# Kernel optimization log

Hardware: AMD Instinct MI355X
Metric: run time of the kernel (lower is better)

## Reference

```python
import jax, jax.numpy as jnp
import numpy as np

N_NODES = 10000
N_EDGES = 120000
F_IN = 66
HEADS = 10
F_HEAD = 66          # GATConv(66, 66, heads=10) -> concat 660
GCN_OUT = F_IN * HEADS * 2  # 1320


def leaky(x, slope):
    return jnp.where(x >= 0, x, slope * x)


def add_self_loops(edge_index, n):
    loops = jnp.arange(n, dtype=edge_index.dtype)
    src = jnp.concatenate([edge_index[0], loops])
    dst = jnp.concatenate([edge_index[1], loops])
    return src, dst


def gat_conv(x, src, dst, W, att_src, att_dst, bias, n):
    # x: [N, F_IN]; W: [F_IN, HEADS*F_HEAD]
    xt = (x @ W).reshape(n, HEADS, F_HEAD)
    a_s = jnp.sum(xt * att_src, axis=-1)   # [N, H]
    a_d = jnp.sum(xt * att_dst, axis=-1)   # [N, H]
    e = leaky(a_s[src] + a_d[dst], 0.2)    # [E, H]
    # segment softmax over destination nodes
    m = jax.ops.segment_max(e, dst, num_segments=n)
    m = jnp.where(jnp.isfinite(m), m, 0.0)
    ex = jnp.exp(e - m[dst])
    s = jax.ops.segment_sum(ex, dst, num_segments=n)
    alpha = ex / jnp.maximum(s[dst], 1e-16)        # [E, H]
    msg = xt[src] * alpha[:, :, None]              # [E, H, F_HEAD]
    out = jax.ops.segment_sum(msg, dst, num_segments=n)
    return out.reshape(n, HEADS * F_HEAD) + bias


def gcn_conv(x, src, dst, W, b, n):
    xt = x @ W                                     # [N, GCN_OUT]
    ones = jnp.ones(src.shape[0], dtype=xt.dtype)
    deg = jax.ops.segment_sum(ones, dst, num_segments=n)
    dinv = jax.lax.rsqrt(jnp.maximum(deg, 1.0))
    norm = dinv[src] * dinv[dst]                   # [E]
    out = jax.ops.segment_sum(xt[src] * norm[:, None], dst, num_segments=n)
    return out + b


def setup_inputs() -> dict:
    key = jax.random.key(0)
    ks = jax.random.split(key, 16)
    x = jax.random.normal(ks[0], (N_NODES, F_IN), dtype=jnp.float32)
    edge_index = jax.random.randint(ks[1], (2, N_EDGES), 0, N_NODES, dtype=jnp.int32)
    sc = 0.05
    p = {
        'x': x,
        'edge_index': edge_index,
        'W_gat': jax.random.normal(ks[2], (F_IN, HEADS * F_HEAD)) * sc,
        'att_src': jax.random.normal(ks[3], (HEADS, F_HEAD)) * sc,
        'att_dst': jax.random.normal(ks[4], (HEADS, F_HEAD)) * sc,
        'b_gat': jnp.zeros((HEADS * F_HEAD,), jnp.float32),
        'W_gcn': jax.random.normal(ks[5], (HEADS * F_HEAD, GCN_OUT)) * sc,
        'b_gcn': jnp.zeros((GCN_OUT,), jnp.float32),
        'W_g1': jax.random.normal(ks[6], (GCN_OUT, 1000)) * sc,
        'b_g1': jnp.zeros((1000,), jnp.float32),
        'W_g2': jax.random.normal(ks[7], (1000, 64)) * sc,
        'b_g2': jnp.zeros((64,), jnp.float32),
        'W_fc1': jax.random.normal(ks[8], (64, 32)) * sc,
        'b_fc1': jnp.zeros((32,), jnp.float32),
        'W_fc2': jax.random.normal(ks[9], (32, 16)) * sc,
        'b_fc2': jnp.zeros((16,), jnp.float32),
        'W_out': jax.random.normal(ks[10], (16, 1)) * sc,
        'b_out': jnp.zeros((1,), jnp.float32),
    }
    return p


def reference(x, edge_index, W_gat, att_src, att_dst, b_gat, W_gcn, b_gcn,
              W_g1, b_g1, W_g2, b_g2, W_fc1, b_fc1, W_fc2, b_fc2, W_out, b_out):
    n = x.shape[0]
    src, dst = add_self_loops(edge_index, n)
    h = gat_conv(x, src, dst, W_gat, att_src, att_dst, b_gat, n)
    h = leaky(h, 0.01)
    h = gcn_conv(h, src, dst, W_gcn, b_gcn, n)
    h = leaky(h, 0.01)
    h = leaky(h @ W_g1 + b_g1, 0.01)   # dropout = identity (eval)
    h = h @ W_g2 + b_g2
    h = leaky(h, 0.01)
    h = leaky(h @ W_fc1 + b_fc1, 0.01)
    h = leaky(h @ W_fc2 + b_fc2, 0.01)
    return h @ W_out + b_out
```

## Files before the change

kernel.cpp:

```cpp
#include <hip/hip_runtime.h>
#include <hip/hip_bf16.h>
#include <math.h>

#define N_NODES 10000
#define MPAD    10112
#define N_EDGESI 120000
#define E_TOT   130000
#define F_INPUT 66
#define HEADS   10
#define F_HEAD  66
#define F_GAT   660
#define F_GCN   1320
#define F_G1    1000
#define F_G2    64

typedef _Float16 half_t;
typedef __attribute__((ext_vector_type(2))) _Float16 f16x2;
typedef __attribute__((ext_vector_type(4))) _Float16 f16x4;
typedef __attribute__((ext_vector_type(8))) _Float16 f16x8;
typedef __attribute__((ext_vector_type(4))) float f32x4;

#define KP_GAT 128
#define NP_GAT 768
#define KP_GCN 704
#define NP_GCN 1408
#define KP_G1  1344
#define NP_G1  1024
#define KP_G2  1024
#define NP_G2  64

__device__ __forceinline__ float lky(float x, float s){ return x >= 0.f ? x : s*x; }

#if defined(__has_builtin)
#if __has_builtin(__builtin_amdgcn_global_load_lds)
#define HAVE_GLL 1
#endif
#endif

#ifdef HAVE_GLL
#define LDSLOAD16(g, l) __builtin_amdgcn_global_load_lds( \
    (const __attribute__((address_space(1))) void*)(g),   \
    (__attribute__((address_space(3))) void*)(l), 16, 0, 0)
#else
#define LDSLOAD16(g, l) (*(f16x8*)(l) = *(const f16x8*)(g))
#endif


__global__ void k_count(const int* __restrict__ ei, int* __restrict__ counts){
    int e = blockIdx.x*256 + threadIdx.x;
    if (e >= E_TOT) return;
    int dst = (e < N_EDGESI) ? ei[N_EDGESI + e] : (e - N_EDGESI);
    atomicAdd(&counts[dst], 1);
}

__global__ __launch_bounds__(1024)
void k_scan(const int* __restrict__ counts, int* __restrict__ offsets,
            float* __restrict__ dinv){
    __shared__ int wsum[16];
    const int lane = threadIdx.x & 63;
    const int wave = threadIdx.x >> 6;
    int carry = 0;
    for (int base = 0; base < N_NODES; base += 1024){
        int i = base + threadIdx.x;
        int v = (i < N_NODES) ? counts[i] : 0;
        if (i < N_NODES) dinv[i] = rsqrtf(fmaxf((float)v, 1.0f));
        int x = v;
        #pragma unroll
        for (int off = 1; off < 64; off <<= 1){
            int y = __shfl_up(x, off, 64);
            if (lane >= off) x += y;
        }
        if (lane == 63) wsum[wave] = x;
        __syncthreads();
        if (wave == 0){
            int w = (lane < 16) ? wsum[lane] : 0;
            #pragma unroll
            for (int off = 1; off < 16; off <<= 1){
                int y = __shfl_up(w, off, 64);
                if (lane >= off) w += y;
            }
            if (lane < 16) wsum[lane] = w;
        }
        __syncthreads();
        int prefix = (wave > 0) ? wsum[wave-1] : 0;
        if (i < N_NODES) offsets[i] = carry + prefix + x - v;
        carry += wsum[15];
        __syncthreads();
    }
    if (threadIdx.x == 0) offsets[N_NODES] = carry;
}

__global__ void k_fill(const int* __restrict__ ei, const int* __restrict__ offsets,
                       int* __restrict__ cursor, int* __restrict__ src_sorted){
    int e = blockIdx.x*256 + threadIdx.x;
    if (e >= E_TOT) return;
    int s, d;
    if (e < N_EDGESI){ s = ei[e]; d = ei[N_EDGESI + e]; }
    else { s = e - N_EDGESI; d = s; }
    int pos = offsets[d] + atomicAdd(&cursor[d], 1);
    src_sorted[pos] = s;
}


__global__ void k_xh(const float* __restrict__ x, half_t* __restrict__ xh){
    int idx = blockIdx.x*256 + threadIdx.x;
    if (idx >= MPAD*KP_GAT) return;
    int r = idx >> 7, c = idx & 127;
    float v = (r < N_NODES && c < F_INPUT) ? x[r*F_INPUT + c] : 0.f;
    xh[idx] = (half_t)v;
}

__global__ void k_wt(const float* __restrict__ W, half_t* __restrict__ WT,
                     int K, int N, int Kp, int Np){
    int idx = blockIdx.x*256 + threadIdx.x;
    if (idx >= Np*Kp) return;
    int n = idx / Kp, k = idx - n*Kp;
    float v = (n < N && k < K) ? W[(size_t)k*N + n] : 0.f;
    WT[idx] = (half_t)v;
}

__global__ __launch_bounds__(256)
void k_hgemm(const half_t* __restrict__ A, const half_t* __restrict__ Bt,
             half_t* __restrict__ C, const float* __restrict__ bias,
             int Nreal, int ldc, int Kp, float slope){
    __shared__ half_t As[128*64];
    __shared__ half_t Bs[64*64];
    const int tid = threadIdx.x;
    const int l = tid & 63;
    const int wid = tid >> 6;
    const int wr = wid >> 1, wc = wid & 1;

    const int gx = gridDim.x;
    const int nwg = gx * gridDim.y;
    const int orig = blockIdx.y * gx + blockIdx.x;
    const int q = nwg >> 3, r8 = nwg & 7;
    const int xcd = orig & 7, lin = orig >> 3;
    const int wgid = (xcd < r8 ? xcd*(q+1) : r8*(q+1) + (xcd-r8)*q) + lin;
    const int bx = wgid % gx, by = wgid / gx;

    const int brow = by * 128;
    const int bcol = bx * 64;

    f32x4 acc[4][2] = {};

    for (int k0 = 0; k0 < Kp; k0 += 64){
        #pragma unroll
        for (int i = 0; i < 4; i++){
            int s = tid + i*256;
            int row = s >> 3, chp = s & 7;
            int ch = chp ^ (row & 7);
            LDSLOAD16(A + (size_t)(brow+row)*Kp + k0 + ch*8, &As[s*8]);
        }
        #pragma unroll
        for (int i = 0; i < 2; i++){
            int s = tid + i*256;
            int row = s >> 3, chp = s & 7;
            int ch = chp ^ (row & 7);
            LDSLOAD16(Bt + (size_t)(bcol+row)*Kp + k0 + ch*8, &Bs[s*8]);
        }
        __syncthreads();
        #pragma unroll
        for (int t = 0; t < 2; t++){
            f16x8 af[4], bf[2];
            #pragma unroll
            for (int m = 0; m < 4; m++){
                int row = wr*64 + m*16 + (l & 15);
                int ch = (t*4 + (l >> 4)) ^ (row & 7);
                af[m] = *(const f16x8*)&As[row*64 + ch*8];
            }
            #pragma unroll
            for (int n = 0; n < 2; n++){
                int row = wc*32 + n*16 + (l & 15);
                int ch = (t*4 + (l >> 4)) ^ (row & 7);
                bf[n] = *(const f16x8*)&Bs[row*64 + ch*8];
            }
            #pragma unroll
            for (int m = 0; m < 4; m++)
                #pragma unroll
                for (int n = 0; n < 2; n++)
                    acc[m][n] = __builtin_amdgcn_mfma_f32_16x16x32_f16(
                        af[m], bf[n], acc[m][n], 0, 0, 0);
        }
        __syncthreads();
    }

    #pragma unroll
    for (int m = 0; m < 4; m++){
        #pragma unroll
        for (int n = 0; n < 2; n++){
            int col = bcol + wc*32 + n*16 + (l & 15);
            if (col >= ldc) continue;
            float bv = (bias && col < Nreal) ? bias[col] : 0.f;
            #pragma unroll
            for (int r = 0; r < 4; r++){
                int rowg = brow + wr*64 + m*16 + ((l >> 4) << 2) + r;
                float v = (col < Nreal) ? acc[m][n][r] + bv : 0.f;
                v = (v >= 0.f) ? v : slope*v;
                C[(size_t)rowg*ldc + col] = (half_t)v;
            }
        }
    }
}


__global__ void k_attn_ad(const half_t* __restrict__ xt,
                          const float* __restrict__ att_src, const float* __restrict__ att_dst,
                          float* __restrict__ a_s, float* __restrict__ a_d){
    int t = blockIdx.x*256 + threadIdx.x;
    if (t >= N_NODES*HEADS) return;
    int n = t / HEADS, h = t - (t/HEADS)*HEADS;
    const half_t* xr = xt + (size_t)n*NP_GAT + h*F_HEAD;
    const float* as = att_src + h*F_HEAD;
    const float* ad = att_dst + h*F_HEAD;
    float s = 0.f, d = 0.f;
    #pragma unroll
    for (int f = 0; f < F_HEAD; f += 2){
        f16x2 v = *(const f16x2*)(xr + f);
        float vx = (float)v.x, vy = (float)v.y;
        s += vx*as[f] + vy*as[f+1];
        d += vx*ad[f] + vy*ad[f+1];
    }
    a_s[t] = s; a_d[t] = d;
}

__global__ void k_softmax(const int* __restrict__ offsets, const int* __restrict__ src_sorted,
                          const float* __restrict__ a_s, const float* __restrict__ a_d,
                          float* __restrict__ e_sorted, float* __restrict__ inv_s){
    int t = blockIdx.x*256 + threadIdx.x;
    if (t >= N_NODES*HEADS) return;
    int n = t / HEADS, h = t - (t/HEADS)*HEADS;
    int b = offsets[n], e = offsets[n+1];
    float ad_n = a_d[t];
    float m = -INFINITY;
    for (int s = b; s < e; s++){
        float v = lky(a_s[src_sorted[s]*HEADS + h] + ad_n, 0.2f);
        e_sorted[(size_t)s*HEADS + h] = v;
        m = fmaxf(m, v);
    }
    float sum = 0.f;
    for (int s = b; s < e; s++){
        float ex = __expf(e_sorted[(size_t)s*HEADS + h] - m);
        e_sorted[(size_t)s*HEADS + h] = ex;
        sum += ex;
    }
    inv_s[t] = 1.0f / fmaxf(sum, 1e-16f);
}

__global__ __launch_bounds__(192)
void k_gat_agg(const int* __restrict__ offsets, const int* __restrict__ src_sorted,
               const float* __restrict__ e_sorted, const float* __restrict__ inv_s,
               const half_t* __restrict__ xt, const float* __restrict__ b_gat,
               half_t* __restrict__ out){
    int n = blockIdx.x, t = threadIdx.x;
    int f0 = 4*t;
    if (t < 165){
        int h0 = f0/F_HEAD;
        int h1 = (f0+1)/F_HEAD;
        int h2 = (f0+2)/F_HEAD;
        int h3 = (f0+3)/F_HEAD;
        int b = offsets[n], e = offsets[n+1];
        float a0=0.f, a1=0.f, a2=0.f, a3=0.f;
        int s = b;
        for (; s + 4 <= e; s += 4){
            int s0 = src_sorted[s],   s1 = src_sorted[s+1];
            int s2 = src_sorted[s+2], s3 = src_sorted[s+3];
            f16x4 v0 = *(const f16x4*)(xt + (size_t)s0*NP_GAT + f0);
            f16x4 v1 = *(const f16x4*)(xt + (size_t)s1*NP_GAT + f0);
            f16x4 v2 = *(const f16x4*)(xt + (size_t)s2*NP_GAT + f0);
            f16x4 v3 = *(const f16x4*)(xt + (size_t)s3*NP_GAT + f0);
            const float* e0 = e_sorted + (size_t)s*HEADS;
            const float* e1 = e0 + HEADS;
            const float* e2 = e0 + 2*HEADS;
            const float* e3 = e0 + 3*HEADS;
            a0 += e0[h0]*(float)v0.x + e1[h0]*(float)v1.x + e2[h0]*(float)v2.x + e3[h0]*(float)v3.x;
            a1 += e0[h1]*(float)v0.y + e1[h1]*(float)v1.y + e2[h1]*(float)v2.y + e3[h1]*(float)v3.y;
            a2 += e0[h2]*(float)v0.z + e1[h2]*(float)v1.z + e2[h2]*(float)v2.z + e3[h2]*(float)v3.z;
            a3 += e0[h3]*(float)v0.w + e1[h3]*(float)v1.w + e2[h3]*(float)v2.w + e3[h3]*(float)v3.w;
        }
        for (; s < e; s++){
            int s0 = src_sorted[s];
            f16x4 v0 = *(const f16x4*)(xt + (size_t)s0*NP_GAT + f0);
            const float* e0 = e_sorted + (size_t)s*HEADS;
            a0 += e0[h0]*(float)v0.x;
            a1 += e0[h1]*(float)v0.y;
            a2 += e0[h2]*(float)v0.z;
            a3 += e0[h3]*(float)v0.w;
        }
        const float* iv = inv_s + n*HEADS;
        f16x4 r;
        r.x = (half_t)lky(a0*iv[h0] + b_gat[f0  ], 0.01f);
        r.y = (half_t)lky(a1*iv[h1] + b_gat[f0+1], 0.01f);
        r.z = (half_t)lky(a2*iv[h2] + b_gat[f0+2], 0.01f);
        r.w = (half_t)lky(a3*iv[h3] + b_gat[f0+3], 0.01f);
        *(f16x4*)(out + (size_t)n*KP_GCN + f0) = r;
    } else if (t < 176){
        f16x4 z = {(half_t)0.f,(half_t)0.f,(half_t)0.f,(half_t)0.f};
        *(f16x4*)(out + (size_t)n*KP_GCN + f0) = z;
    }
}


__global__ __launch_bounds__(192)
void k_gcn_pre(const int* __restrict__ offsets, const int* __restrict__ src_sorted,
               const float* __restrict__ dinv, const half_t* __restrict__ h1,
               half_t* __restrict__ agg){
    int n = blockIdx.x, t = threadIdx.x;
    int f0 = 4*t;
    if (t < 165){
        int b = offsets[n], e = offsets[n+1];
        float a0=0.f, a1=0.f, a2=0.f, a3=0.f;
        int s = b;
        for (; s + 4 <= e; s += 4){
            int s0 = src_sorted[s],   s1 = src_sorted[s+1];
            int s2 = src_sorted[s+2], s3 = src_sorted[s+3];
            float n0 = dinv[s0], n1 = dinv[s1], n2 = dinv[s2], n3 = dinv[s3];
            f16x4 v0 = *(const f16x4*)(h1 + (size_t)s0*KP_GCN + f0);
            f16x4 v1 = *(const f16x4*)(h1 + (size_t)s1*KP_GCN + f0);
            f16x4 v2 = *(const f16x4*)(h1 + (size_t)s2*KP_GCN + f0);
            f16x4 v3 = *(const f16x4*)(h1 + (size_t)s3*KP_GCN + f0);
            a0 += n0*(float)v0.x + n1*(float)v1.x + n2*(float)v2.x + n3*(float)v3.x;
            a1 += n0*(float)v0.y + n1*(float)v1.y + n2*(float)v2.y + n3*(float)v3.y;
            a2 += n0*(float)v0.z + n1*(float)v1.z + n2*(float)v2.z + n3*(float)v3.z;
            a3 += n0*(float)v0.w + n1*(float)v1.w + n2*(float)v2.w + n3*(float)v3.w;
        }
        for (; s < e; s++){
            int s0 = src_sorted[s];
            float n0 = dinv[s0];
            f16x4 v0 = *(const f16x4*)(h1 + (size_t)s0*KP_GCN + f0);
            a0 += n0*(float)v0.x;
            a1 += n0*(float)v0.y;
            a2 += n0*(float)v0.z;
            a3 += n0*(float)v0.w;
        }
        float dn = dinv[n];
        f16x4 r;
        r.x = (half_t)(dn*a0); r.y = (half_t)(dn*a1);
        r.z = (half_t)(dn*a2); r.w = (half_t)(dn*a3);
        *(f16x4*)(agg + (size_t)n*KP_GCN + f0) = r;
    } else if (t < 176){
        f16x4 z = {(half_t)0.f,(half_t)0.f,(half_t)0.f,(half_t)0.f};
        *(f16x4*)(agg + (size_t)n*KP_GCN + f0) = z;
    }
}

__global__ __launch_bounds__(256)
void k_tail(const half_t* __restrict__ h4,
            const float* __restrict__ Wfc1, const float* __restrict__ bfc1,
            const float* __restrict__ Wfc2, const float* __restrict__ bfc2,
            const float* __restrict__ Wout, const float* __restrict__ bout,
            float* __restrict__ out){
    __shared__ float W1[64*32];
    __shared__ float W2[32*16];
    __shared__ float Wo[16];
    __shared__ float b1[32];
    __shared__ float b2[16];
    __shared__ float r1[8][32];
    __shared__ float r2[8][16];
    int tid = threadIdx.x;
    for (int i = tid; i < 64*32; i += 256) W1[i] = Wfc1[i];
    for (int i = tid; i < 32*16; i += 256) W2[i] = Wfc2[i];
    if (tid < 16) Wo[tid] = Wout[tid];
    if (tid < 32) b1[tid] = bfc1[tid];
    if (tid < 16) b2[tid] = bfc2[tid];
    __syncthreads();
    int g = tid >> 5, j = tid & 31;
    int node = blockIdx.x*8 + g;
    const half_t* hr = h4 + (size_t)node*F_G2;
    float acc = 0.f;
    #pragma unroll 8
    for (int i = 0; i < 64; i++) acc += (float)hr[i]*W1[i*32 + j];
    r1[g][j] = lky(acc + b1[j], 0.01f);
    __syncthreads();
    if (j < 16){
        float a2 = 0.f;
        #pragma unroll
        for (int i = 0; i < 32; i++) a2 += r1[g][i]*W2[i*16 + j];
        r2[g][j] = lky(a2 + b2[j], 0.01f);
    }
    __syncthreads();
    if (j == 0){
        float a3 = 0.f;
        #pragma unroll
        for (int i = 0; i < 16; i++) a3 += r2[g][i]*Wo[i];
        out[node] = a3 + bout[0];
    }
}


extern "C" void kernel_launch(void* const* d_in, const int* in_sizes, int n_in,
                              void* d_out, int out_size, void* d_ws, size_t ws_size,
                              hipStream_t stream){
    const float* x       = (const float*)d_in[0];
    const int*   ei      = (const int*)  d_in[1];
    const float* W_gat   = (const float*)d_in[2];
    const float* att_src = (const float*)d_in[3];
    const float* att_dst = (const float*)d_in[4];
    const float* b_gat   = (const float*)d_in[5];
    const float* W_gcn   = (const float*)d_in[6];
    const float* b_gcn   = (const float*)d_in[7];
    const float* W_g1    = (const float*)d_in[8];
    const float* b_g1    = (const float*)d_in[9];
    const float* W_g2    = (const float*)d_in[10];
    const float* b_g2    = (const float*)d_in[11];
    const float* W_fc1   = (const float*)d_in[12];
    const float* b_fc1   = (const float*)d_in[13];
    const float* W_fc2   = (const float*)d_in[14];
    const float* b_fc2   = (const float*)d_in[15];
    const float* W_out   = (const float*)d_in[16];
    const float* b_out   = (const float*)d_in[17];
    float* out = (float*)d_out;
    char* ws = (char*)d_ws;

    size_t off = 0;
    auto alloc = [&](size_t bytes){ size_t o = off; off += (bytes + 255) & ~(size_t)255; return o; };
    size_t o_counts = alloc(N_NODES*4);
    size_t o_cursor = alloc(N_NODES*4);
    size_t o_offs   = alloc((N_NODES+1)*4);
    size_t o_as     = alloc(N_NODES*HEADS*4);
    size_t o_ad     = alloc(N_NODES*HEADS*4);
    size_t o_invs   = alloc(N_NODES*HEADS*4);
    size_t o_dinv   = alloc(N_NODES*4);
    size_t o_srcs   = alloc(E_TOT*4);
    size_t o_esrt   = alloc((size_t)E_TOT*HEADS*4);
    size_t o_xh     = alloc((size_t)MPAD*KP_GAT*2);
    size_t o_xt     = alloc((size_t)MPAD*NP_GAT*2);
    size_t o_h1     = alloc((size_t)N_NODES*KP_GCN*2);
    size_t o_agg    = alloc((size_t)MPAD*KP_GCN*2);
    size_t o_h2     = alloc((size_t)MPAD*KP_G1*2);
    size_t o_h3     = alloc((size_t)MPAD*KP_G2*2);
    size_t o_h4     = alloc((size_t)MPAD*F_G2*2);
    size_t o_wgatT  = alloc((size_t)NP_GAT*KP_GAT*2);
    size_t o_wgcnT  = alloc((size_t)NP_GCN*KP_GCN*2);
    size_t o_wg1T   = alloc((size_t)NP_G1*KP_G1*2);
    size_t o_wg2T   = alloc((size_t)NP_G2*KP_G2*2);

    int*    counts  = (int*)(ws + o_counts);
    int*    cursor  = (int*)(ws + o_cursor);
    int*    offsets = (int*)(ws + o_offs);
    float*  a_s     = (float*)(ws + o_as);
    float*  a_d     = (float*)(ws + o_ad);
    float*  inv_s   = (float*)(ws + o_invs);
    float*  dinv    = (float*)(ws + o_dinv);
    int*    src_srt = (int*)(ws + o_srcs);
    float*  e_srt   = (float*)(ws + o_esrt);
    half_t* xh      = (half_t*)(ws + o_xh);
    half_t* xt_h    = (half_t*)(ws + o_xt);
    half_t* h1h     = (half_t*)(ws + o_h1);
    half_t* aggh    = (half_t*)(ws + o_agg);
    half_t* h2h     = (half_t*)(ws + o_h2);
    half_t* h3h     = (half_t*)(ws + o_h3);
    half_t* h4h     = (half_t*)(ws + o_h4);
    half_t* WgatT   = (half_t*)(ws + o_wgatT);
    half_t* WgcnT   = (half_t*)(ws + o_wgcnT);
    half_t* Wg1T    = (half_t*)(ws + o_wg1T);
    half_t* Wg2T    = (half_t*)(ws + o_wg2T);

    hipMemsetAsync(ws + o_counts, 0, o_offs - o_counts, stream);
    k_count<<<(E_TOT+255)/256, 256, 0, stream>>>(ei, counts);
    k_scan<<<1, 1024, 0, stream>>>(counts, offsets, dinv);
    k_fill<<<(E_TOT+255)/256, 256, 0, stream>>>(ei, offsets, cursor, src_srt);

    k_xh<<<(MPAD*KP_GAT+255)/256, 256, 0, stream>>>(x, xh);
    k_wt<<<(NP_GAT*KP_GAT+255)/256, 256, 0, stream>>>(W_gat, WgatT, F_INPUT, F_GAT, KP_GAT, NP_GAT);
    k_wt<<<(NP_GCN*KP_GCN+255)/256, 256, 0, stream>>>(W_gcn, WgcnT, F_GAT, F_GCN, KP_GCN, NP_GCN);
    k_wt<<<(NP_G1*KP_G1+255)/256, 256, 0, stream>>>(W_g1, Wg1T, F_GCN, F_G1, KP_G1, NP_G1);
    k_wt<<<(NP_G2*KP_G2+255)/256, 256, 0, stream>>>(W_g2, Wg2T, F_G1, F_G2, KP_G2, NP_G2);

    k_hgemm<<<dim3(NP_GAT/64, MPAD/128), 256, 0, stream>>>(
        xh, WgatT, xt_h, nullptr, F_GAT, NP_GAT, KP_GAT, 1.0f);
    k_attn_ad<<<(N_NODES*HEADS+255)/256, 256, 0, stream>>>(xt_h, att_src, att_dst, a_s, a_d);
    k_softmax<<<(N_NODES*HEADS+255)/256, 256, 0, stream>>>(offsets, src_srt, a_s, a_d, e_srt, inv_s);
    k_gat_agg<<<N_NODES, 192, 0, stream>>>(offsets, src_srt, e_srt, inv_s, xt_h, b_gat, h1h);

    k_gcn_pre<<<N_NODES, 192, 0, stream>>>(offsets, src_srt, dinv, h1h, aggh);
    k_hgemm<<<dim3(NP_GCN/64, MPAD/128), 256, 0, stream>>>(
        aggh, WgcnT, h2h, b_gcn, F_GCN, KP_G1, KP_GCN, 0.01f);

    k_hgemm<<<dim3(NP_G1/64, MPAD/128), 256, 0, stream>>>(
        h2h, Wg1T, h3h, b_g1, F_G1, KP_G2, KP_G1, 0.01f);
    k_hgemm<<<dim3(NP_G2/64, MPAD/128), 256, 0, stream>>>(
        h3h, Wg2T, h4h, b_g2, F_G2, F_G2, KP_G2, 0.01f);
    k_tail<<<N_NODES/8, 256, 0, stream>>>(h4h, W_fc1, b_fc1, W_fc2, b_fc2,
                                          W_out, b_out, out);
}
```

Baseline: 331.3 us.

## Fuse weight packing into one launch and fuse final GEMM with MLP tail

Merges the five separate fp16 conversion/transpose kernels into one 2D-grid packing kernel. It also fuses the last 1000→64 GEMM with the three small dense layers, keeping the 64-wide activations in shared memory instead of writing and re-reading them. The goal is fewer kernel launches and less global traffic. The trade-off is that the fused tail GEMM runs on only 79 workgroups and the per-node MLP runs on half the threads with a serial loop, which could underuse the GPU.

```diff
diff --git a/kernel.cpp b/kernel.cpp
--- a/kernel.cpp
+++ b/kernel.cpp
@@ -102,21 +102,51 @@
 }
 
 
-__global__ void k_xh(const float* __restrict__ x, half_t* __restrict__ xh){
-    int idx = blockIdx.x*256 + threadIdx.x;
-    if (idx >= MPAD*KP_GAT) return;
-    int r = idx >> 7, c = idx & 127;
-    float v = (r < N_NODES && c < F_INPUT) ? x[r*F_INPUT + c] : 0.f;
-    xh[idx] = (half_t)v;
-}
-
-__global__ void k_wt(const float* __restrict__ W, half_t* __restrict__ WT,
-                     int K, int N, int Kp, int Np){
-    int idx = blockIdx.x*256 + threadIdx.x;
-    if (idx >= Np*Kp) return;
-    int n = idx / Kp, k = idx - n*Kp;
-    float v = (n < N && k < K) ? W[(size_t)k*N + n] : 0.f;
-    WT[idx] = (half_t)v;
+#define C_XH   (MPAD*KP_GAT)
+#define C_WGAT (NP_GAT*KP_GAT)
+#define C_WGCN (NP_GCN*KP_GCN)
+#define C_WG1  (NP_G1*KP_G1)
+#define C_WG2  (NP_G2*KP_G2)
+#define PACK_BX ((C_WG1 + 1023) / 1024)
+
+__global__ void k_packy(const float* __restrict__ x,
+                        const float* __restrict__ Wgat, const float* __restrict__ Wgcn,
+                        const float* __restrict__ Wg1,  const float* __restrict__ Wg2,
+                        half_t* __restrict__ xh, half_t* __restrict__ WgatT,
+                        half_t* __restrict__ WgcnT, half_t* __restrict__ Wg1T,
+                        half_t* __restrict__ Wg2T){
+    int base = blockIdx.x*1024 + threadIdx.x;
+    int y = blockIdx.y;
+    #pragma unroll
+    for (int p = 0; p < 4; p++){
+        int idx = base + p*256;
+        if (y == 0){
+            if (idx < C_XH){
+                int r = idx >> 7, c = idx & 127;
+                xh[idx] = (half_t)((r < N_NODES && c < F_INPUT) ? x[r*F_INPUT + c] : 0.f);
+            }
+        } else if (y == 1){
+            if (idx < C_WGAT){
+                int n = idx >> 7, k = idx & 127;
+                WgatT[idx] = (half_t)((n < F_GAT && k < F_INPUT) ? Wgat[k*F_GAT + n] : 0.f);
+            }
+        } else if (y == 2){
+            if (idx < C_WGCN){
+                int n = idx / KP_GCN, k = idx - n*KP_GCN;
+                WgcnT[idx] = (half_t)((n < F_GCN && k < F_GAT) ? Wgcn[k*F_GCN + n] : 0.f);
+            }
+        } else if (y == 3){
+            if (idx < C_WG1){
+                int n = idx / KP_G1, k = idx - n*KP_G1;
+                Wg1T[idx] = (half_t)((n < F_G1 && k < F_GCN) ? Wg1[k*F_G1 + n] : 0.f);
+            }
+        } else {
+            if (idx < C_WG2){
+                int n = idx >> 10, k = idx & 1023;
+                Wg2T[idx] = (half_t)((n < F_G2 && k < F_G1) ? Wg2[k*F_G2 + n] : 0.f);
+            }
+        }
+    }
 }
 
 __global__ __launch_bounds__(256)
@@ -199,6 +229,124 @@
                 C[(size_t)rowg*ldc + col] = (half_t)v;
             }
         }
+    }
+}
+
+__global__ __launch_bounds__(256)
+void k_g2tail(const half_t* __restrict__ A, const half_t* __restrict__ Bt,
+              const float* __restrict__ bias,
+              const float* __restrict__ Wfc1, const float* __restrict__ bfc1,
+              const float* __restrict__ Wfc2, const float* __restrict__ bfc2,
+              const float* __restrict__ Wout, const float* __restrict__ bout,
+              float* __restrict__ out){
+    __shared__ half_t As[128*64];
+    __shared__ half_t Bs[64*64];
+    __shared__ float h4s[128][65];
+    __shared__ float W1s[64*32];
+    __shared__ float W2s[32*16];
+    __shared__ float Wos[16];
+    __shared__ float b1s[32];
+    __shared__ float b2s[16];
+    const int tid = threadIdx.x;
+
+    for (int i = tid; i < 64*32; i += 256) W1s[i] = Wfc1[i];
+    for (int i = tid; i < 32*16; i += 256) W2s[i] = Wfc2[i];
+    if (tid < 16) Wos[tid] = Wout[tid];
+    if (tid < 32) b1s[tid] = bfc1[tid];
+    if (tid < 16) b2s[tid] = bfc2[tid];
+
+    const int l = tid & 63;
+    const int wid = tid >> 6;
+    const int wr = wid >> 1, wc = wid & 1;
+
+    const int nwg = gridDim.y;
+    const int orig = blockIdx.y;
+    const int q = nwg >> 3, r8 = nwg & 7;
+    const int xcd = orig & 7, lin = orig >> 3;
+    const int wgid = (xcd < r8 ? xcd*(q+1) : r8*(q+1) + (xcd-r8)*q) + lin;
+    const int brow = wgid * 128;
+
+    f32x4 acc[4][2] = {};
+
+    for (int k0 = 0; k0 < KP_G2; k0 += 64){
+        #pragma unroll
+        for (int i = 0; i < 4; i++){
+            int s = tid + i*256;
+            int row = s >> 3, chp = s & 7;
+            int ch = chp ^ (row & 7);
+            LDSLOAD16(A + (size_t)(brow+row)*KP_G2 + k0 + ch*8, &As[s*8]);
+        }
+        #pragma unroll
+        for (int i = 0; i < 2; i++){
+            int s = tid + i*256;
+            int row = s >> 3, chp = s & 7;
+            int ch = chp ^ (row & 7);
+            LDSLOAD16(Bt + (size_t)row*KP_G2 + k0 + ch*8, &Bs[s*8]);
+        }
+        __syncthreads();
+        #pragma unroll
+        for (int t = 0; t < 2; t++){
+            f16x8 af[4], bf[2];
+            #pragma unroll
+            for (int m = 0; m < 4; m++){
+                int row = wr*64 + m*16 + (l & 15);
+                int ch = (t*4 + (l >> 4)) ^ (row & 7);
+                af[m] = *(const f16x8*)&As[row*64 + ch*8];
+            }
+            #pragma unroll
+            for (int n = 0; n < 2; n++){
+                int row = wc*32 + n*16 + (l & 15);
+                int ch = (t*4 + (l >> 4)) ^ (row & 7);
+                bf[n] = *(const f16x8*)&Bs[row*64 + ch*8];
+            }
+            #pragma unroll
+            for (int m = 0; m < 4; m++)
+                #pragma unroll
+                for (int n = 0; n < 2; n++)
+                    acc[m][n] = __builtin_amdgcn_mfma_f32_16x16x32_f16(
+                        af[m], bf[n], acc[m][n], 0, 0, 0);
+        }
+        __syncthreads();
+    }
+
+    #pragma unroll
+    for (int m = 0; m < 4; m++){
+        #pragma unroll
+        for (int n = 0; n < 2; n++){
+            int col = wc*32 + n*16 + (l & 15);
+            float bv = bias[col];
+            #pragma unroll
+            for (int r = 0; r < 4; r++){
+                int row = wr*64 + m*16 + ((l >> 4) << 2) + r;
+                float v = acc[m][n][r] + bv;
+                h4s[row][col] = (v >= 0.f) ? v : 0.01f*v;
+            }
+        }
+    }
+    __syncthreads();
+
+    if (tid < 128){
+        int node = brow + tid;
+        float h1v[32];
+        #pragma unroll 4
+        for (int j = 0; j < 32; j++){
+            float a = b1s[j];
+            #pragma unroll 8
+            for (int i = 0; i < 64; i++) a += h4s[tid][i]*W1s[i*32 + j];
+            h1v[j] = lky(a, 0.01f);
+        }
+        float h2v[16];
+        #pragma unroll
+        for (int j = 0; j < 16; j++){
+            float a = b2s[j];
+            #pragma unroll
+            for (int i = 0; i < 32; i++) a += h1v[i]*W2s[i*16 + j];
+            h2v[j] = lky(a, 0.01f);
+        }
+        float a3 = bout[0];
+        #pragma unroll
+        for (int i = 0; i < 16; i++) a3 += h2v[i]*Wos[i];
+        if (node < N_NODES) out[node] = a3;
     }
 }
 
@@ -343,49 +491,6 @@
     }
 }
 
-__global__ __launch_bounds__(256)
-void k_tail(const half_t* __restrict__ h4,
-            const float* __restrict__ Wfc1, const float* __restrict__ bfc1,
-            const float* __restrict__ Wfc2, const float* __restrict__ bfc2,
-            const float* __restrict__ Wout, const float* __restrict__ bout,
-            float* __restrict__ out){
-    __shared__ float W1[64*32];
-    __shared__ float W2[32*16];
-    __shared__ float Wo[16];
-    __shared__ float b1[32];
-    __shared__ float b2[16];
-    __shared__ float r1[8][32];
-    __shared__ float r2[8][16];
-    int tid = threadIdx.x;
-    for (int i = tid; i < 64*32; i += 256) W1[i] = Wfc1[i];
-    for (int i = tid; i < 32*16; i += 256) W2[i] = Wfc2[i];
-    if (tid < 16) Wo[tid] = Wout[tid];
-    if (tid < 32) b1[tid] = bfc1[tid];
-    if (tid < 16) b2[tid] = bfc2[tid];
-    __syncthreads();
-    int g = tid >> 5, j = tid & 31;
-    int node = blockIdx.x*8 + g;
-    const half_t* hr = h4 + (size_t)node*F_G2;
-    float acc = 0.f;
-    #pragma unroll 8
-    for (int i = 0; i < 64; i++) acc += (float)hr[i]*W1[i*32 + j];
-    r1[g][j] = lky(acc + b1[j], 0.01f);
-    __syncthreads();
-    if (j < 16){
-        float a2 = 0.f;
-        #pragma unroll
-        for (int i = 0; i < 32; i++) a2 += r1[g][i]*W2[i*16 + j];
-        r2[g][j] = lky(a2 + b2[j], 0.01f);
-    }
-    __syncthreads();
-    if (j == 0){
-        float a3 = 0.f;
-        #pragma unroll
-        for (int i = 0; i < 16; i++) a3 += r2[g][i]*Wo[i];
-        out[node] = a3 + bout[0];
-    }
-}
-
 
 extern "C" void kernel_launch(void* const* d_in, const int* in_sizes, int n_in,
                               void* d_out, int out_size, void* d_ws, size_t ws_size,
@@ -428,7 +533,6 @@
     size_t o_agg    = alloc((size_t)MPAD*KP_GCN*2);
     size_t o_h2     = alloc((size_t)MPAD*KP_G1*2);
     size_t o_h3     = alloc((size_t)MPAD*KP_G2*2);
-    size_t o_h4     = alloc((size_t)MPAD*F_G2*2);
     size_t o_wgatT  = alloc((size_t)NP_GAT*KP_GAT*2);
     size_t o_wgcnT  = alloc((size_t)NP_GCN*KP_GCN*2);
     size_t o_wg1T   = alloc((size_t)NP_G1*KP_G1*2);
@@ -449,7 +553,6 @@
     half_t* aggh    = (half_t*)(ws + o_agg);
     half_t* h2h     = (half_t*)(ws + o_h2);
     half_t* h3h     = (half_t*)(ws + o_h3);
-    half_t* h4h     = (half_t*)(ws + o_h4);
     half_t* WgatT   = (half_t*)(ws + o_wgatT);
     half_t* WgcnT   = (half_t*)(ws + o_wgcnT);
     half_t* Wg1T    = (half_t*)(ws + o_wg1T);
@@ -460,11 +563,8 @@
     k_scan<<<1, 1024, 0, stream>>>(counts, offsets, dinv);
     k_fill<<<(E_TOT+255)/256, 256, 0, stream>>>(ei, offsets, cursor, src_srt);
 
-    k_xh<<<(MPAD*KP_GAT+255)/256, 256, 0, stream>>>(x, xh);
-    k_wt<<<(NP_GAT*KP_GAT+255)/256, 256, 0, stream>>>(W_gat, WgatT, F_INPUT, F_GAT, KP_GAT, NP_GAT);
-    k_wt<<<(NP_GCN*KP_GCN+255)/256, 256, 0, stream>>>(W_gcn, WgcnT, F_GAT, F_GCN, KP_GCN, NP_GCN);
-    k_wt<<<(NP_G1*KP_G1+255)/256, 256, 0, stream>>>(W_g1, Wg1T, F_GCN, F_G1, KP_G1, NP_G1);
-    k_wt<<<(NP_G2*KP_G2+255)/256, 256, 0, stream>>>(W_g2, Wg2T, F_G1, F_G2, KP_G2, NP_G2);
+    k_packy<<<dim3(PACK_BX, 5), 256, 0, stream>>>(x, W_gat, W_gcn, W_g1, W_g2,
+                                                  xh, WgatT, WgcnT, Wg1T, Wg2T);
 
     k_hgemm<<<dim3(NP_GAT/64, MPAD/128), 256, 0, stream>>>(
         xh, WgatT, xt_h, nullptr, F_GAT, NP_GAT, KP_GAT, 1.0f);
@@ -478,8 +578,6 @@
 
     k_hgemm<<<dim3(NP_G1/64, MPAD/128), 256, 0, stream>>>(
         h2h, Wg1T, h3h, b_g1, F_G1, KP_G2, KP_G1, 0.01f);
-    k_hgemm<<<dim3(NP_G2/64, MPAD/128), 256, 0, stream>>>(
-        h3h, Wg2T, h4h, b_g2, F_G2, F_G2, KP_G2, 0.01f);
-    k_tail<<<N_NODES/8, 256, 0, stream>>>(h4h, W_fc1, b_fc1, W_fc2, b_fc2,
-                                          W_out, b_out, out);
-}
+    k_g2tail<<<dim3(1, MPAD/128), 256, 0, stream>>>(
+        h3h, Wg2T, b_g2, W_fc1, b_fc1, W_fc2, b_fc2, W_out, b_out, out);
+}
```

Result: slower. 343.6 us (+3.7%).
